# Performance work log

Measured on AMD Instinct MI355X. Metric: run time of the kernel, lower is better.

Reference implementation:

```python
import jax, jax.numpy as jnp
import numpy as np

M, N, IN, H, NC = 2048, 64, 16, 256, 64
OUT = 3 * NC
NUM_LAYERS = 2


def _lstm_layer(x, Wih, Whh, bih, bhh):
    # x: (M, T, F); Wih: (4H, F); Whh: (4H, H). Torch gate order: i, f, g, o.
    xg = jnp.einsum('mtf,gf->mtg', x, Wih) + bih + bhh  # (M, T, 4H)
    h0 = jnp.zeros((x.shape[0], Whh.shape[1]), x.dtype)

    def step(carry, xt):
        h, c = carry
        gates = xt + h @ Whh.T
        i, f, g, o = jnp.split(gates, 4, axis=-1)
        c = jax.nn.sigmoid(f) * c + jax.nn.sigmoid(i) * jnp.tanh(g)
        h = jax.nn.sigmoid(o) * jnp.tanh(c)
        return (h, c), h

    (_, _), hs = jax.lax.scan(step, (h0, h0), jnp.swapaxes(xg, 0, 1))
    return jnp.swapaxes(hs, 0, 1)  # (M, T, H)


def setup_inputs() -> dict:
    key = jax.random.key(0)
    ks = jax.random.split(key, 12)
    s = 1.0 / np.sqrt(H)
    d = {
        'z': jax.random.normal(ks[0], (M, N, IN), jnp.float32),
        'Wih0': jax.random.normal(ks[1], (4 * H, IN), jnp.float32) * s,
        'Whh0': jax.random.normal(ks[2], (4 * H, H), jnp.float32) * s,
        'bih0': jax.random.normal(ks[3], (4 * H,), jnp.float32) * s,
        'bhh0': jax.random.normal(ks[4], (4 * H,), jnp.float32) * s,
        'Wih1': jax.random.normal(ks[5], (4 * H, H), jnp.float32) * s,
        'Whh1': jax.random.normal(ks[6], (4 * H, H), jnp.float32) * s,
        'bih1': jax.random.normal(ks[7], (4 * H,), jnp.float32) * s,
        'bhh1': jax.random.normal(ks[8], (4 * H,), jnp.float32) * s,
        'fcW': jax.random.normal(ks[9], (OUT, H), jnp.float32) * 0.02,
        'fcb': jax.random.normal(ks[10], (OUT,), jnp.float32) * 0.02,
    }
    return d


def reference(z, Wih0, Whh0, bih0, bhh0, Wih1, Whh1, bih1, bhh1, fcW, fcb):
    h = _lstm_layer(z, Wih0, Whh0, bih0, bhh0)
    h = _lstm_layer(h, Wih1, Whh1, bih1, bhh1)
    y = jnp.einsum('mth,oh->mto', h, fcW) + fcb  # (M, N, 3*NC)

    gammas = jax.nn.softmax(y[..., :NC], axis=2)
    sigmas = jnp.exp(y[..., NC:2 * NC])
    mus = y[..., 2 * NC:]

    key = jax.random.key(42)
    k1, k2 = jax.random.split(key)
    idx = jax.random.categorical(k1, jnp.log(gammas), axis=-1)  # (M, N)
    chosen_mu = jnp.take_along_axis(mus, idx[..., None], axis=2)     # (M, N, 1)
    chosen_sig = jnp.take_along_axis(sigmas, idx[..., None], axis=2)
    eps = jax.random.normal(k2, chosen_mu.shape, jnp.float32)
    x_pred = jax.lax.stop_gradient(chosen_mu + chosen_sig * eps)  # Normal.sample (no grad)

    kern_exp = (x_pred - mus) ** 2                         # broadcast repeat over NC
    kernels = jnp.exp(-0.5 * kern_exp) / sigmas ** 2
    kernels = kernels / ((2.0 * jnp.pi) ** (N / 2) * sigmas ** N)
    x_cond_prob = jnp.einsum('mtc,mtc->mt', gammas, kernels)  # (M, N)
    return x_pred, x_cond_prob
```

## Files before the change

### kernel.cpp

```cpp
#include <hip/hip_runtime.h>
#include <stdint.h>
#include <stddef.h>

#define Mdim 2048
#define Tdim 64
#define INdim 16
#define Hdim 256
#define NCdim 64
#define NUG 64
#define HSLAB (256 * 2048)
#define RSLOTS 16

typedef __attribute__((ext_vector_type(8))) short s16x8;
typedef __attribute__((ext_vector_type(4))) float f32x4;

#define PANEL_US (3 * 16 * 8 * 512)
#define SPOFF 65536
#define BFRAG_US (3 * 8 * 3 * 512)

#define OFF_BFRAG 0
#define OFF_WZ    1179648
#define OFF_BB    (OFF_WZ + 64 * 256)
#define OFF_WFCP  (OFF_BB + 64 * 32)
#define OFF_H0P   (OFF_WFCP + 256 * 64 * 4)
#define OFF_C0    (OFF_H0P + 1572864)
#define OFF_C1    (OFF_C0 + HSLAB)
#define OFF_RINGF (OFF_C1 + HSLAB)
#define OFF_RING2 (OFF_RINGF + 12582912)
#define WS_TOT    (OFF_RING2 + RSLOTS * HSLAB)

#define ROTL32(v, s) (((v) << (s)) | ((v) >> (32 - (s))))

__host__ __device__ inline void tf2x32(uint32_t k0, uint32_t k1, uint32_t x0, uint32_t x1,
                                       uint32_t* o0, uint32_t* o1) {
  uint32_t ks2 = k0 ^ k1 ^ 0x1BD11BDAu;
  x0 += k0; x1 += k1;
  x0 += x1; x1 = ROTL32(x1, 13); x1 ^= x0;
  x0 += x1; x1 = ROTL32(x1, 15); x1 ^= x0;
  x0 += x1; x1 = ROTL32(x1, 26); x1 ^= x0;
  x0 += x1; x1 = ROTL32(x1, 6);  x1 ^= x0;
  x0 += k1; x1 += ks2 + 1u;
  x0 += x1; x1 = ROTL32(x1, 17); x1 ^= x0;
  x0 += x1; x1 = ROTL32(x1, 29); x1 ^= x0;
  x0 += x1; x1 = ROTL32(x1, 16); x1 ^= x0;
  x0 += x1; x1 = ROTL32(x1, 24); x1 ^= x0;
  x0 += ks2; x1 += k0 + 2u;
  x0 += x1; x1 = ROTL32(x1, 13); x1 ^= x0;
  x0 += x1; x1 = ROTL32(x1, 15); x1 ^= x0;
  x0 += x1; x1 = ROTL32(x1, 26); x1 ^= x0;
  x0 += x1; x1 = ROTL32(x1, 6);  x1 ^= x0;
  x0 += k0; x1 += k1 + 3u;
  x0 += x1; x1 = ROTL32(x1, 17); x1 ^= x0;
  x0 += x1; x1 = ROTL32(x1, 29); x1 ^= x0;
  x0 += x1; x1 = ROTL32(x1, 16); x1 ^= x0;
  x0 += x1; x1 = ROTL32(x1, 24); x1 ^= x0;
  x0 += k1; x1 += ks2 + 4u;
  x0 += x1; x1 = ROTL32(x1, 13); x1 ^= x0;
  x0 += x1; x1 = ROTL32(x1, 15); x1 ^= x0;
  x0 += x1; x1 = ROTL32(x1, 26); x1 ^= x0;
  x0 += x1; x1 = ROTL32(x1, 6);  x1 ^= x0;
  x0 += ks2; x1 += k0 + 5u;
  *o0 = x0; *o1 = x1;
}

__device__ inline uint32_t random_bits32(uint32_t ka, uint32_t kb, uint32_t p) {
  uint32_t a, b;
  tf2x32(ka, kb, 0u, p, &a, &b);
  return a ^ b;
}

__device__ inline float bits_to_u01(uint32_t bits) {
  return __uint_as_float((bits >> 9) | 0x3f800000u) - 1.0f;
}

__device__ inline float sigm_fast(float x) { return 1.0f / (1.0f + __expf(-x)); }

__device__ inline float erfinv_f32(float x) {
  float w = -log1pf(-x * x);
  float p;
  if (w < 5.0f) {
    w -= 2.5f;
    p = 2.81022636e-08f;
    p = fmaf(p, w, 3.43273939e-07f);
    p = fmaf(p, w, -3.5233877e-06f);
    p = fmaf(p, w, -4.39150654e-06f);
    p = fmaf(p, w, 0.00021858087f);
    p = fmaf(p, w, -0.00125372503f);
    p = fmaf(p, w, -0.00417768164f);
    p = fmaf(p, w, 0.246640727f);
    p = fmaf(p, w, 1.50140941f);
  } else {
    w = sqrtf(w) - 3.0f;
    p = -0.000200214257f;
    p = fmaf(p, w, 0.000100950558f);
    p = fmaf(p, w, 0.00134934322f);
    p = fmaf(p, w, -0.00367342844f);
    p = fmaf(p, w, 0.00573950773f);
    p = fmaf(p, w, -0.0076224613f);
    p = fmaf(p, w, 0.00943887047f);
    p = fmaf(p, w, 1.00167406f);
    p = fmaf(p, w, 2.83297682f);
  }
  return p * x;
}

__device__ inline void mdn_head(float yg, float ysg, float ym, int lane, uint32_t rid,
                                uint32_t k1a, uint32_t k1b, uint32_t k2a, uint32_t k2b,
                                float* __restrict__ out) {
  uint32_t pp = rid * (uint32_t)NCdim + (uint32_t)lane;
  uint32_t bits = random_bits32(k1a, k1b, pp);
  float u01 = bits_to_u01(bits);
  const float tinyf = 1.17549435e-38f;
  float uu = fmaxf(tinyf, u01 + tinyf);
  float gum = -logf(-logf(uu));
  float val = gum + yg;
  int idx = lane;
#pragma unroll
  for (int s = 1; s < 64; s <<= 1) {
    float ov = __shfl_xor(val, s);
    int oi = __shfl_xor(idx, s);
    if (ov > val || (ov == val && oi < idx)) { val = ov; idx = oi; }
  }
  float mu_sel = __shfl(ym, idx);
  float s_sel = __shfl(ysg, idx);

  uint32_t ebits = random_bits32(k2a, k2b, rid);
  float ue = bits_to_u01(ebits);
  const float lo = __uint_as_float(0xBF7FFFFFu);
  float un2 = fmaxf(lo, ue * 2.0f + lo);
  float eps = 1.41421356f * erfinv_f32(un2);

  float x_pred = mu_sel + expf(s_sel) * eps;

  float mx = yg;
#pragma unroll
  for (int s = 1; s < 64; s <<= 1) mx = fmaxf(mx, __shfl_xor(mx, s));
  float se = expf(yg - mx);
#pragma unroll
  for (int s = 1; s < 64; s <<= 1) se += __shfl_xor(se, s);
  float d = x_pred - ym;
  float lk = -0.5f * d * d - 66.0f * ysg - 58.812066f;
  float ts = expf(yg - mx + lk);
#pragma unroll
  for (int s = 1; s < 64; s <<= 1) ts += __shfl_xor(ts, s);
  float prob = ts / se;

  if (lane == 0) {
    out[rid] = x_pred;
    out[(size_t)Mdim * Tdim + rid] = prob;
  }
}

__device__ __host__ inline unsigned short bf16_trunc(float x) {
  union { float f; uint32_t u; } c; c.f = x;
  return (unsigned short)(c.u >> 16);
}
__device__ __host__ inline float bf16_tof(unsigned short s) {
  union { float f; uint32_t u; } c; c.u = ((uint32_t)s) << 16;
  return c.f;
}

__global__ void vfpg_prep(const float* __restrict__ Wih0, const float* __restrict__ Whh0,
                          const float* __restrict__ Wih1, const float* __restrict__ Whh1,
                          const float* __restrict__ fcW, const float* __restrict__ bih0,
                          const float* __restrict__ bhh0, const float* __restrict__ bih1,
                          const float* __restrict__ bhh1, float* __restrict__ ws) {
  int i0 = blockIdx.x * blockDim.x + threadIdx.x;
  int n = blockDim.x * gridDim.x;
  unsigned short* BF = (unsigned short*)(ws + OFF_BFRAG);
  for (int i = i0; i < 64 * 3 * 8 * 512; i += n) {
    int ug = i / 12288, r = i % 12288;
    int cls = r / 4096, r2 = r % 4096;
    int kt = r2 >> 9, pos = r2 & 511;
    int l = pos >> 3, e = pos & 7;
    int n16 = l & 15, lg = l >> 4;
    int k = kt * 32 + lg * 8 + e;
    int ul = n16 >> 2, ty = n16 & 3;
    int gd = ty * 256 + ug * 4 + ul;
    const float* W = (cls == 0) ? Whh0 : ((cls == 1) ? Wih1 : Whh1);
    float w = W[gd * 256 + k];
    unsigned short s0 = bf16_trunc(w);
    float r1 = w - bf16_tof(s0);
    unsigned short s1 = bf16_trunc(r1);
    unsigned short s2 = bf16_trunc(r1 - bf16_tof(s1));
    size_t base = ((size_t)(ug * 3 + cls) * 8 + kt) * (3 * 512) + pos;
    BF[base] = s0;
    BF[base + 512] = s1;
    BF[base + 1024] = s2;
  }
  for (int i = i0; i < 64 * 256; i += n) {
    int ug = i >> 8, k = (i >> 4) & 15, g = i & 15;
    int gd = (g & 3) * 256 + ug * 4 + (g >> 2);
    ws[OFF_WZ + i] = Wih0[gd * INdim + k];
  }
  for (int i = i0; i < 64 * 32; i += n) {
    int ug = i >> 5, r = i & 31, g = r & 15;
    int gd = (g & 3) * 256 + ug * 4 + (g >> 2);
    ws[OFF_BB + i] = (r < 16) ? (bih0[gd] + bhh0[gd]) : (bih1[gd] + bhh1[gd]);
  }
  float4* wfcp = (float4*)(ws + OFF_WFCP);
  for (int o = i0; o < 256 * 64; o += n) {
    int k = o >> 6, c = o & 63;
    wfcp[o] = make_float4(fcW[c * Hdim + k], fcW[(64 + c) * Hdim + k],
                          fcW[(128 + c) * Hdim + k], 0.0f);
  }
}

__device__ inline void cell1s(float gi, float gf, float gg, float go, float cold,
                              float* cn, float* hn) {
  float si = sigm_fast(gi), sf = sigm_fast(gf);
  float tg = fmaf(2.0f, sigm_fast(2.0f * gg), -1.0f);
  float so = sigm_fast(go);
  float cc = fmaf(sf, cold, si * tg);
  *cn = cc;
  *hn = so * fmaf(2.0f, sigm_fast(2.0f * cc), -1.0f);
}

#define GBS 17

template <int MODE>
__launch_bounds__(256, 3)
__global__ void vfpg_step(const float* __restrict__ z, const float* __restrict__ ws,
                          float* __restrict__ wsm, int t) {
  __shared__ unsigned short lB[2 * 8 * 2 * 512];
  __shared__ float gbuf[256 * GBS];
  __shared__ float lz[256];
  __shared__ float lbias[32];

  const int tid = threadIdx.x;
  const int rg = blockIdx.x & 7, ug = blockIdx.x >> 3;
  const int mb = rg * 256;
  const int lane = tid & 63, wid = tid >> 6;

  {
    const unsigned short* BG = (const unsigned short*)(ws + OFF_BFRAG) + (size_t)ug * BFRAG_US;
    s16x8* dst = (s16x8*)lB;
    for (int i = tid; i < 2 * 8 * 2 * 64; i += 256) {
      int ck = i >> 7, sp = (i >> 6) & 1, v = i & 63;
      dst[i] = *(const s16x8*)(BG + ((size_t)ck * 3 + sp) * 512 + v * 8);
    }
    if (tid < 64) ((float4*)lz)[tid] = ((const float4*)(ws + OFF_WZ + ug * 256))[tid];
    if (tid < 32) lbias[tid] = ws[OFF_BB + ug * 32 + tid];
  }
  __syncthreads();

  f32x4 aL0[4], aL1[4];
#pragma unroll
  for (int i = 0; i < 4; i++) {
    aL0[i] = (f32x4)0.0f;
    aL1[i] = (f32x4)0.0f;
  }

  if (MODE >= 1) {
    const unsigned short* p0 = (const unsigned short*)(ws + OFF_H0P) +
                               ((size_t)((t - 1) & 1) * 8 + rg) * PANEL_US;
    const unsigned short* p1 = (const unsigned short*)(ws + OFF_RINGF) +
                               ((size_t)((t - 2) & 15) * 8 + rg) * PANEL_US;
    const unsigned short* BG2 = (const unsigned short*)(ws + OFF_BFRAG) + (size_t)ug * BFRAG_US;
    const bool doH1 = (t >= 2);
    const s16x8* pLB = (const s16x8*)lB;

    s16x8 Ab0[6], Ab1[6];
    {
      size_t fb = ((size_t)(wid * 4) * 8 + 0) * 512 + lane * 8;
      Ab0[0] = *(const s16x8*)(p0 + fb);
      Ab0[1] = *(const s16x8*)(p0 + fb + SPOFF);
      Ab0[2] = *(const s16x8*)(p0 + fb + 2 * SPOFF);
      if (doH1) {
        Ab0[3] = *(const s16x8*)(p1 + fb);
        Ab0[4] = *(const s16x8*)(p1 + fb + SPOFF);
        Ab0[5] = *(const s16x8*)(p1 + fb + 2 * SPOFF);
      }
    }

#pragma unroll 1
    for (int kt = 0; kt < 8; kt++) {
      s16x8 bL0s0, bL0s1, bL0s2, bIs0, bIs1, bIs2, bHs0, bHs1, bHs2;
      if (MODE == 1) {
        bL0s0 = pLB[(kt * 2 + 0) * 64 + lane];
        bL0s1 = pLB[(kt * 2 + 1) * 64 + lane];
        bL0s2 = *(const s16x8*)(BG2 + ((size_t)kt * 3 + 2) * 512 + lane * 8);
      }
      bIs0 = pLB[((8 + kt) * 2 + 0) * 64 + lane];
      bIs1 = pLB[((8 + kt) * 2 + 1) * 64 + lane];
      bIs2 = *(const s16x8*)(BG2 + ((size_t)(8 + kt) * 3 + 2) * 512 + lane * 8);
      if (doH1) {
        bHs0 = *(const s16x8*)(BG2 + ((size_t)(16 + kt) * 3 + 0) * 512 + lane * 8);
        bHs1 = *(const s16x8*)(BG2 + ((size_t)(16 + kt) * 3 + 1) * 512 + lane * 8);
        bHs2 = *(const s16x8*)(BG2 + ((size_t)(16 + kt) * 3 + 2) * 512 + lane * 8);
      }
#pragma unroll
      for (int i = 0; i < 4; i++) {
        s16x8* cur = (i & 1) ? Ab1 : Ab0;
        s16x8* nxt = (i & 1) ? Ab0 : Ab1;
        int nkt = (i < 3) ? kt : kt + 1;
        int ni = (i < 3) ? (i + 1) : 0;
        if (nkt < 8) {
          size_t fb = ((size_t)(wid * 4 + ni) * 8 + nkt) * 512 + lane * 8;
          nxt[0] = *(const s16x8*)(p0 + fb);
          nxt[1] = *(const s16x8*)(p0 + fb + SPOFF);
          nxt[2] = *(const s16x8*)(p0 + fb + 2 * SPOFF);
          if (doH1) {
            nxt[3] = *(const s16x8*)(p1 + fb);
            nxt[4] = *(const s16x8*)(p1 + fb + SPOFF);
            nxt[5] = *(const s16x8*)(p1 + fb + 2 * SPOFF);
          }
        }
        s16x8 a0 = cur[0], a1 = cur[1], a2 = cur[2];
        if (MODE == 1) {
          aL0[i] = __builtin_amdgcn_mfma_f32_16x16x32_bf16(a0, bL0s0, aL0[i], 0, 0, 0);
          aL0[i] = __builtin_amdgcn_mfma_f32_16x16x32_bf16(a0, bL0s1, aL0[i], 0, 0, 0);
          aL0[i] = __builtin_amdgcn_mfma_f32_16x16x32_bf16(a1, bL0s0, aL0[i], 0, 0, 0);
          aL0[i] = __builtin_amdgcn_mfma_f32_16x16x32_bf16(a1, bL0s1, aL0[i], 0, 0, 0);
          aL0[i] = __builtin_amdgcn_mfma_f32_16x16x32_bf16(a0, bL0s2, aL0[i], 0, 0, 0);
          aL0[i] = __builtin_amdgcn_mfma_f32_16x16x32_bf16(a2, bL0s0, aL0[i], 0, 0, 0);
        }
        aL1[i] = __builtin_amdgcn_mfma_f32_16x16x32_bf16(a0, bIs0, aL1[i], 0, 0, 0);
        aL1[i] = __builtin_amdgcn_mfma_f32_16x16x32_bf16(a0, bIs1, aL1[i], 0, 0, 0);
        aL1[i] = __builtin_amdgcn_mfma_f32_16x16x32_bf16(a1, bIs0, aL1[i], 0, 0, 0);
        aL1[i] = __builtin_amdgcn_mfma_f32_16x16x32_bf16(a1, bIs1, aL1[i], 0, 0, 0);
        aL1[i] = __builtin_amdgcn_mfma_f32_16x16x32_bf16(a0, bIs2, aL1[i], 0, 0, 0);
        aL1[i] = __builtin_amdgcn_mfma_f32_16x16x32_bf16(a2, bIs0, aL1[i], 0, 0, 0);
        if (doH1) {
          s16x8 c0 = cur[3], c1 = cur[4], c2 = cur[5];
          aL1[i] = __builtin_amdgcn_mfma_f32_16x16x32_bf16(c0, bHs0, aL1[i], 0, 0, 0);
          aL1[i] = __builtin_amdgcn_mfma_f32_16x16x32_bf16(c0, bHs1, aL1[i], 0, 0, 0);
          aL1[i] = __builtin_amdgcn_mfma_f32_16x16x32_bf16(c1, bHs0, aL1[i], 0, 0, 0);
          aL1[i] = __builtin_amdgcn_mfma_f32_16x16x32_bf16(c1, bHs1, aL1[i], 0, 0, 0);
          aL1[i] = __builtin_amdgcn_mfma_f32_16x16x32_bf16(c0, bHs2, aL1[i], 0, 0, 0);
          aL1[i] = __builtin_amdgcn_mfma_f32_16x16x32_bf16(c2, bHs0, aL1[i], 0, 0, 0);
        }
      }
    }
  }

  float* c0w = wsm + OFF_C0;
  float* c1w = wsm + OFF_C1;
  const int mloc = tid;
  const int m = mb + mloc;
  const int mtc = mloc >> 4, mrowc = mloc & 15;
  const int ktw = ug >> 3;
  const int lgw = (ug & 7) >> 1;
  const int ebase = (ug * 4) & 7;
  const int lww = lgw * 16 + mrowc;
  const size_t fo = ((size_t)mtc * 8 + ktw) * 512 + lww * 8 + ebase;

  if (MODE <= 1) {
    if (MODE == 1) {
      int col = lane & 15, rb2 = (lane >> 4) * 4;
#pragma unroll
      for (int i = 0; i < 4; i++) {
        int mt = wid * 4 + i;
#pragma unroll
        for (int j = 0; j < 4; j++)
          gbuf[(mt * 16 + rb2 + j) * GBS + col] = aL0[i][j];
      }
    }
    __syncthreads();
    float zr[16];
#pragma unroll
    for (int f4 = 0; f4 < 4; f4++)
      *(float4*)&zr[f4 * 4] = *(const float4*)&z[(size_t)m * 1024 + t * 16 + f4 * 4];
    float g16[16];
#pragma unroll
    for (int gg = 0; gg < 16; gg++)
      g16[gg] = lbias[gg] + ((MODE == 1) ? gbuf[mloc * GBS + gg] : 0.0f);
#pragma unroll
    for (int f = 0; f < 16; f++) {
      float zv = zr[f];
      float4 w0 = *(const float4*)&lz[f * 16 + 0];
      float4 w1 = *(const float4*)&lz[f * 16 + 4];
      float4 w2 = *(const float4*)&lz[f * 16 + 8];
      float4 w3 = *(const float4*)&lz[f * 16 + 12];
      g16[0] = fmaf(zv, w0.x, g16[0]);  g16[1] = fmaf(zv, w0.y, g16[1]);
      g16[2] = fmaf(zv, w0.z, g16[2]);  g16[3] = fmaf(zv, w0.w, g16[3]);
      g16[4] = fmaf(zv, w1.x, g16[4]);  g16[5] = fmaf(zv, w1.y, g16[5]);
      g16[6] = fmaf(zv, w1.z, g16[6]);  g16[7] = fmaf(zv, w1.w, g16[7]);
      g16[8] = fmaf(zv, w2.x, g16[8]);  g16[9] = fmaf(zv, w2.y, g16[9]);
      g16[10] = fmaf(zv, w2.z, g16[10]); g16[11] = fmaf(zv, w2.w, g16[11]);
      g16[12] = fmaf(zv, w3.x, g16[12]); g16[13] = fmaf(zv, w3.y, g16[13]);
      g16[14] = fmaf(zv, w3.z, g16[14]); g16[15] = fmaf(zv, w3.w, g16[15]);
    }
    unsigned short* wp = (unsigned short*)(wsm + OFF_H0P) +
                         ((size_t)(t & 1) * 8 + rg) * PANEL_US;
    short sp0[4], sp1[4], sp2[4];
#pragma unroll
    for (int ul = 0; ul < 4; ul++) {
      int u = ug * 4 + ul;
      size_t cidx = (size_t)u * 2048 + m;
      float cold = (MODE == 1) ? c0w[cidx] : 0.0f;
      float cn, hn;
      cell1s(g16[ul * 4 + 0], g16[ul * 4 + 1], g16[ul * 4 + 2], g16[ul * 4 + 3], cold, &cn, &hn);
      c0w[cidx] = cn;
      unsigned short s0 = bf16_trunc(hn);
      float r1 = hn - bf16_tof(s0);
      unsigned short s1 = bf16_trunc(r1);
      unsigned short s2 = bf16_trunc(r1 - bf16_tof(s1));
      sp0[ul] = (short)s0; sp1[ul] = (short)s1; sp2[ul] = (short)s2;
    }
    *(short4*)&wp[fo]             = make_short4(sp0[0], sp0[1], sp0[2], sp0[3]);
    *(short4*)&wp[fo + SPOFF]     = make_short4(sp1[0], sp1[1], sp1[2], sp1[3]);
    *(short4*)&wp[fo + 2 * SPOFF] = make_short4(sp2[0], sp2[1], sp2[2], sp2[3]);
    __syncthreads();
  }

  if (MODE >= 1) {
    {
      int col = lane & 15, rb2 = (lane >> 4) * 4;
#pragma unroll
      for (int i = 0; i < 4; i++) {
        int mt = wid * 4 + i;
#pragma unroll
        for (int j = 0; j < 4; j++)
          gbuf[(mt * 16 + rb2 + j) * GBS + col] = aL1[i][j];
      }
    }
    __syncthreads();
    int slot = (t - 1) & 15;
    unsigned short* rp = (unsigned short*)(wsm + OFF_RINGF) +
                         ((size_t)slot * 8 + rg) * PANEL_US;
    float* r2 = wsm + OFF_RING2 + (size_t)slot * HSLAB;
    float h4[4];
    short sp0[4], sp1[4], sp2[4];
#pragma unroll
    for (int ul = 0; ul < 4; ul++) {
      int gg = ul * 4;
      float gi = lbias[16 + gg + 0] + gbuf[mloc * GBS + gg + 0];
      float gf = lbias[16 + gg + 1] + gbuf[mloc * GBS + gg + 1];
      float gt = lbias[16 + gg + 2] + gbuf[mloc * GBS + gg + 2];
      float go = lbias[16 + gg + 3] + gbuf[mloc * GBS + gg + 3];
      int u = ug * 4 + ul;
      size_t cidx = (size_t)u * 2048 + m;
      float cold = (t >= 2) ? c1w[cidx] : 0.0f;
      float cn, hn;
      cell1s(gi, gf, gt, go, cold, &cn, &hn);
      c1w[cidx] = cn;
      h4[ul] = hn;
      unsigned short s0 = bf16_trunc(hn);
      float r1v = hn - bf16_tof(s0);
      unsigned short s1 = bf16_trunc(r1v);
      unsigned short s2 = bf16_trunc(r1v - bf16_tof(s1));
      sp0[ul] = (short)s0; sp1[ul] = (short)s1; sp2[ul] = (short)s2;
    }
    *(short4*)&rp[fo]             = make_short4(sp0[0], sp0[1], sp0[2], sp0[3]);
    *(short4*)&rp[fo + SPOFF]     = make_short4(sp1[0], sp1[1], sp1[2], sp1[3]);
    *(short4*)&rp[fo + 2 * SPOFF] = make_short4(sp2[0], sp2[1], sp2[2], sp2[3]);
    *(float4*)&r2[(size_t)m * 256 + ug * 4] = make_float4(h4[0], h4[1], h4[2], h4[3]);
  }
}

__launch_bounds__(512, 2)
__global__ void vfpg_head(const float* __restrict__ ws, const float* __restrict__ fcb,
                          float* __restrict__ out, int tbase,
                          uint32_t k1a, uint32_t k1b, uint32_t k2a, uint32_t k2b) {
  __shared__ __align__(16) float hsw[8][8][Hdim];
  const int tid = threadIdx.x;
  const int lane = tid & 63, wid = tid >> 6;
  const int rb8 = blockIdx.x * 8 + wid;
  const int slot = rb8 >> 8;
  const int mbase = (rb8 & 255) * 8;

  const float* r2 = ws + OFF_RING2 + (size_t)slot * HSLAB + (size_t)mbase * 256;
  const float4* WFCP = (const float4*)(ws + OFF_WFCP);

#pragma unroll
  for (int rr = 0; rr < 8; rr++)
    *(float4*)&hsw[wid][rr][lane * 4] = *(const float4*)&r2[rr * 256 + lane * 4];
  __builtin_amdgcn_s_waitcnt(0);

  float yg[8], ys[8], ym[8];
#pragma unroll
  for (int rr = 0; rr < 8; rr++) {
    yg[rr] = fcb[lane]; ys[rr] = fcb[64 + lane]; ym[rr] = fcb[128 + lane];
  }
#pragma unroll 2
  for (int k4 = 0; k4 < 64; k4++) {
    float4 h4[8];
#pragma unroll
    for (int rr = 0; rr < 8; rr++) h4[rr] = *(const float4*)&hsw[wid][rr][k4 * 4];
#pragma unroll
    for (int j = 0; j < 4; j++) {
      float4 w = WFCP[(k4 * 4 + j) * 64 + lane];
#pragma unroll
      for (int rr = 0; rr < 8; rr++) {
        float hv = (&h4[rr].x)[j];
        yg[rr] = fmaf(hv, w.x, yg[rr]);
        ys[rr] = fmaf(hv, w.y, ys[rr]);
        ym[rr] = fmaf(hv, w.z, ym[rr]);
      }
    }
  }
  int tt = tbase + slot;
#pragma unroll 1
  for (int rr = 0; rr < 8; rr++) {
    uint32_t rid = (uint32_t)(mbase + rr) * Tdim + (uint32_t)tt;
    mdn_head(yg[rr], ys[rr], ym[rr], lane, rid, k1a, k1b, k2a, k2b, out);
  }
}

extern "C" void kernel_launch(void* const* d_in, const int* in_sizes, int n_in,
                              void* d_out, int out_size, void* d_ws, size_t ws_size,
                              hipStream_t stream) {
  const float* z    = (const float*)d_in[0];
  const float* Wih0 = (const float*)d_in[1];
  const float* Whh0 = (const float*)d_in[2];
  const float* bih0 = (const float*)d_in[3];
  const float* bhh0 = (const float*)d_in[4];
  const float* Wih1 = (const float*)d_in[5];
  const float* Whh1 = (const float*)d_in[6];
  const float* bih1 = (const float*)d_in[7];
  const float* bhh1 = (const float*)d_in[8];
  const float* fcW  = (const float*)d_in[9];
  const float* fcb  = (const float*)d_in[10];
  float* ws = (float*)d_ws;
  float* out = (float*)d_out;

  if (ws_size < (size_t)WS_TOT * sizeof(float)) return;

  vfpg_prep<<<dim3(512), dim3(256), 0, stream>>>(
      Wih0, Whh0, Wih1, Whh1, fcW, bih0, bhh0, bih1, bhh1, ws);

  uint32_t k1a, k1b, k2a, k2b;
  tf2x32(0u, 42u, 0u, 0u, &k1a, &k1b);
  tf2x32(0u, 42u, 0u, 1u, &k2a, &k2b);

  vfpg_step<0><<<dim3(512), dim3(256), 0, stream>>>(z, ws, ws, 0);
  for (int t = 1; t <= 63; t++) {
    vfpg_step<1><<<dim3(512), dim3(256), 0, stream>>>(z, ws, ws, t);
    if (t == 16 || t == 32 || t == 48) {
      vfpg_head<<<dim3(512), dim3(512), 0, stream>>>(ws, fcb, out, t - 16,
                                                     k1a, k1b, k2a, k2b);
    }
  }
  vfpg_step<2><<<dim3(512), dim3(256), 0, stream>>>(z, ws, ws, 64);
  vfpg_head<<<dim3(512), dim3(512), 0, stream>>>(ws, fcb, out, 48, k1a, k1b, k2a, k2b);
}
```

Baseline: 2.081 ms.

## Merge two unit-groups per block so A panels are reused across gate columns

Each step block now handles two unit-groups (512 threads, 256 blocks) instead of one, so every A-fragment load from the hidden-state panels feeds MFMAs for both groups. This halves global A traffic per output. All B fragments, including the split-2 and recurrent-layer-1 weights that were previously read from global each k-step, are now staged in shared memory through a union buffer reused for the gate scratch. The cost is higher shared-memory use (about 130 KB per block), fewer and larger blocks, lower occupancy, and an extra barrier before the gate buffer is reused.

After: 2.069 ms. About the same (-0.6%).

```diff
diff --git a/kernel.cpp b/kernel.cpp
--- a/kernel.cpp
+++ b/kernel.cpp
@@ -216,53 +216,67 @@
   *hn = so * fmaf(2.0f, sigm_fast(2.0f * cc), -1.0f);
 }
 
-#define GBS 17
+#define GBS2 33
 
 template <int MODE>
-__launch_bounds__(256, 3)
+__launch_bounds__(512, 2)
 __global__ void vfpg_step(const float* __restrict__ z, const float* __restrict__ ws,
                           float* __restrict__ wsm, int t) {
-  __shared__ unsigned short lB[2 * 8 * 2 * 512];
-  __shared__ float gbuf[256 * GBS];
-  __shared__ float lz[256];
-  __shared__ float lbias[32];
+  __shared__ unsigned short lB01[2 * 2 * 8 * 2 * 512];
+  __shared__ __align__(16) unsigned char uni[81920];
+  __shared__ float lz[2 * 256];
+  __shared__ float lbias[64];
 
   const int tid = threadIdx.x;
-  const int rg = blockIdx.x & 7, ug = blockIdx.x >> 3;
+  const int rg = blockIdx.x & 7, ugc = blockIdx.x >> 3;
   const int mb = rg * 256;
   const int lane = tid & 63, wid = tid >> 6;
+  float* gbuf = (float*)uni;
 
   {
-    const unsigned short* BG = (const unsigned short*)(ws + OFF_BFRAG) + (size_t)ug * BFRAG_US;
-    s16x8* dst = (s16x8*)lB;
-    for (int i = tid; i < 2 * 8 * 2 * 64; i += 256) {
-      int ck = i >> 7, sp = (i >> 6) & 1, v = i & 63;
-      dst[i] = *(const s16x8*)(BG + ((size_t)ck * 3 + sp) * 512 + v * 8);
-    }
-    if (tid < 64) ((float4*)lz)[tid] = ((const float4*)(ws + OFF_WZ + ug * 256))[tid];
-    if (tid < 32) lbias[tid] = ws[OFF_BB + ug * 32 + tid];
+    const unsigned short* BF = (const unsigned short*)(ws + OFF_BFRAG);
+    const unsigned short* BG0 = BF + (size_t)(ugc * 2 + 0) * BFRAG_US;
+    const unsigned short* BG1 = BF + (size_t)(ugc * 2 + 1) * BFRAG_US;
+    for (int i = tid; i < 2 * 4608; i += 512) {
+      int ugl = i / 4608;
+      int r = i % 4608;
+      int cls = r / 1536;
+      int r2 = r % 1536;
+      int kt = r2 / 192;
+      int sp = (r2 / 64) % 3;
+      int v = r2 & 63;
+      const unsigned short* src = (ugl ? BG1 : BG0) + ((size_t)(cls * 8 + kt) * 3 + sp) * 512 + v * 8;
+      s16x8 val = *(const s16x8*)src;
+      if (cls < 2 && sp < 2) {
+        ((s16x8*)lB01)[((((ugl * 2 + cls) * 8 + kt) * 2 + sp)) * 64 + v] = val;
+      } else {
+        int str = (cls == 2) ? (2 + sp) : cls;
+        ((s16x8*)uni)[(((ugl * 5 + str) * 8 + kt)) * 64 + v] = val;
+      }
+    }
+    if (tid < 128) ((float4*)lz)[tid] = ((const float4*)(ws + OFF_WZ + (ugc * 2) * 256))[tid];
+    if (tid < 64) lbias[tid] = ws[OFF_BB + (ugc * 2) * 32 + tid];
   }
   __syncthreads();
 
-  f32x4 aL0[4], aL1[4];
-#pragma unroll
-  for (int i = 0; i < 4; i++) {
-    aL0[i] = (f32x4)0.0f;
-    aL1[i] = (f32x4)0.0f;
-  }
+  f32x4 aL0[2][2], aL1[2][2];
+#pragma unroll
+  for (int i = 0; i < 2; i++)
+#pragma unroll
+    for (int u = 0; u < 2; u++) { aL0[i][u] = (f32x4)0.0f; aL1[i][u] = (f32x4)0.0f; }
 
   if (MODE >= 1) {
     const unsigned short* p0 = (const unsigned short*)(ws + OFF_H0P) +
                                ((size_t)((t - 1) & 1) * 8 + rg) * PANEL_US;
     const unsigned short* p1 = (const unsigned short*)(ws + OFF_RINGF) +
                                ((size_t)((t - 2) & 15) * 8 + rg) * PANEL_US;
-    const unsigned short* BG2 = (const unsigned short*)(ws + OFF_BFRAG) + (size_t)ug * BFRAG_US;
     const bool doH1 = (t >= 2);
-    const s16x8* pLB = (const s16x8*)lB;
+    const s16x8* pL = (const s16x8*)lB01;
+    const s16x8* pU = (const s16x8*)uni;
 
     s16x8 Ab0[6], Ab1[6];
     {
-      size_t fb = ((size_t)(wid * 4) * 8 + 0) * 512 + lane * 8;
+      size_t fb = ((size_t)(wid * 2) * 8 + 0) * 512 + lane * 8;
       Ab0[0] = *(const s16x8*)(p0 + fb);
       Ab0[1] = *(const s16x8*)(p0 + fb + SPOFF);
       Ab0[2] = *(const s16x8*)(p0 + fb + 2 * SPOFF);
@@ -275,28 +289,31 @@
 
 #pragma unroll 1
     for (int kt = 0; kt < 8; kt++) {
-      s16x8 bL0s0, bL0s1, bL0s2, bIs0, bIs1, bIs2, bHs0, bHs1, bHs2;
-      if (MODE == 1) {
-        bL0s0 = pLB[(kt * 2 + 0) * 64 + lane];
-        bL0s1 = pLB[(kt * 2 + 1) * 64 + lane];
-        bL0s2 = *(const s16x8*)(BG2 + ((size_t)kt * 3 + 2) * 512 + lane * 8);
+      s16x8 bL0s0[2], bL0s1[2], bL0s2[2], bIs0[2], bIs1[2], bIs2[2], bHs0[2], bHs1[2], bHs2[2];
+#pragma unroll
+      for (int u = 0; u < 2; u++) {
+        if (MODE == 1) {
+          bL0s0[u] = pL[(((u * 2 + 0) * 8 + kt) * 2 + 0) * 64 + lane];
+          bL0s1[u] = pL[(((u * 2 + 0) * 8 + kt) * 2 + 1) * 64 + lane];
+          bL0s2[u] = pU[((u * 5 + 0) * 8 + kt) * 64 + lane];
+        }
+        bIs0[u] = pL[(((u * 2 + 1) * 8 + kt) * 2 + 0) * 64 + lane];
+        bIs1[u] = pL[(((u * 2 + 1) * 8 + kt) * 2 + 1) * 64 + lane];
+        bIs2[u] = pU[((u * 5 + 1) * 8 + kt) * 64 + lane];
+        if (doH1) {
+          bHs0[u] = pU[((u * 5 + 2) * 8 + kt) * 64 + lane];
+          bHs1[u] = pU[((u * 5 + 3) * 8 + kt) * 64 + lane];
+          bHs2[u] = pU[((u * 5 + 4) * 8 + kt) * 64 + lane];
+        }
       }
-      bIs0 = pLB[((8 + kt) * 2 + 0) * 64 + lane];
-      bIs1 = pLB[((8 + kt) * 2 + 1) * 64 + lane];
-      bIs2 = *(const s16x8*)(BG2 + ((size_t)(8 + kt) * 3 + 2) * 512 + lane * 8);
-      if (doH1) {
-        bHs0 = *(const s16x8*)(BG2 + ((size_t)(16 + kt) * 3 + 0) * 512 + lane * 8);
-        bHs1 = *(const s16x8*)(BG2 + ((size_t)(16 + kt) * 3 + 1) * 512 + lane * 8);
-        bHs2 = *(const s16x8*)(BG2 + ((size_t)(16 + kt) * 3 + 2) * 512 + lane * 8);
-      }
-#pragma unroll
-      for (int i = 0; i < 4; i++) {
+#pragma unroll
+      for (int i = 0; i < 2; i++) {
         s16x8* cur = (i & 1) ? Ab1 : Ab0;
         s16x8* nxt = (i & 1) ? Ab0 : Ab1;
-        int nkt = (i < 3) ? kt : kt + 1;
-        int ni = (i < 3) ? (i + 1) : 0;
+        int nkt = (i < 1) ? kt : kt + 1;
+        int ni = (i < 1) ? 1 : 0;
         if (nkt < 8) {
-          size_t fb = ((size_t)(wid * 4 + ni) * 8 + nkt) * 512 + lane * 8;
+          size_t fb = ((size_t)(wid * 2 + ni) * 8 + nkt) * 512 + lane * 8;
           nxt[0] = *(const s16x8*)(p0 + fb);
           nxt[1] = *(const s16x8*)(p0 + fb + SPOFF);
           nxt[2] = *(const s16x8*)(p0 + fb + 2 * SPOFF);
@@ -307,37 +324,43 @@
           }
         }
         s16x8 a0 = cur[0], a1 = cur[1], a2 = cur[2];
-        if (MODE == 1) {
-          aL0[i] = __builtin_amdgcn_mfma_f32_16x16x32_bf16(a0, bL0s0, aL0[i], 0, 0, 0);
-          aL0[i] = __builtin_amdgcn_mfma_f32_16x16x32_bf16(a0, bL0s1, aL0[i], 0, 0, 0);
-          aL0[i] = __builtin_amdgcn_mfma_f32_16x16x32_bf16(a1, bL0s0, aL0[i], 0, 0, 0);
-          aL0[i] = __builtin_amdgcn_mfma_f32_16x16x32_bf16(a1, bL0s1, aL0[i], 0, 0, 0);
-          aL0[i] = __builtin_amdgcn_mfma_f32_16x16x32_bf16(a0, bL0s2, aL0[i], 0, 0, 0);
-          aL0[i] = __builtin_amdgcn_mfma_f32_16x16x32_bf16(a2, bL0s0, aL0[i], 0, 0, 0);
-        }
-        aL1[i] = __builtin_amdgcn_mfma_f32_16x16x32_bf16(a0, bIs0, aL1[i], 0, 0, 0);
-        aL1[i] = __builtin_amdgcn_mfma_f32_16x16x32_bf16(a0, bIs1, aL1[i], 0, 0, 0);
-        aL1[i] = __builtin_amdgcn_mfma_f32_16x16x32_bf16(a1, bIs0, aL1[i], 0, 0, 0);
-        aL1[i] = __builtin_amdgcn_mfma_f32_16x16x32_bf16(a1, bIs1, aL1[i], 0, 0, 0);
-        aL1[i] = __builtin_amdgcn_mfma_f32_16x16x32_bf16(a0, bIs2, aL1[i], 0, 0, 0);
-        aL1[i] = __builtin_amdgcn_mfma_f32_16x16x32_bf16(a2, bIs0, aL1[i], 0, 0, 0);
-        if (doH1) {
-          s16x8 c0 = cur[3], c1 = cur[4], c2 = cur[5];
-          aL1[i] = __builtin_amdgcn_mfma_f32_16x16x32_bf16(c0, bHs0, aL1[i], 0, 0, 0);
-          aL1[i] = __builtin_amdgcn_mfma_f32_16x16x32_bf16(c0, bHs1, aL1[i], 0, 0, 0);
-          aL1[i] = __builtin_amdgcn_mfma_f32_16x16x32_bf16(c1, bHs0, aL1[i], 0, 0, 0);
-          aL1[i] = __builtin_amdgcn_mfma_f32_16x16x32_bf16(c1, bHs1, aL1[i], 0, 0, 0);
-          aL1[i] = __builtin_amdgcn_mfma_f32_16x16x32_bf16(c0, bHs2, aL1[i], 0, 0, 0);
-          aL1[i] = __builtin_amdgcn_mfma_f32_16x16x32_bf16(c2, bHs0, aL1[i], 0, 0, 0);
+#pragma unroll
+        for (int u = 0; u < 2; u++) {
+          if (MODE == 1) {
+            aL0[i][u] = __builtin_amdgcn_mfma_f32_16x16x32_bf16(a0, bL0s0[u], aL0[i][u], 0, 0, 0);
+            aL0[i][u] = __builtin_amdgcn_mfma_f32_16x16x32_bf16(a0, bL0s1[u], aL0[i][u], 0, 0, 0);
+            aL0[i][u] = __builtin_amdgcn_mfma_f32_16x16x32_bf16(a1, bL0s0[u], aL0[i][u], 0, 0, 0);
+            aL0[i][u] = __builtin_amdgcn_mfma_f32_16x16x32_bf16(a1, bL0s1[u], aL0[i][u], 0, 0, 0);
+            aL0[i][u] = __builtin_amdgcn_mfma_f32_16x16x32_bf16(a0, bL0s2[u], aL0[i][u], 0, 0, 0);
+            aL0[i][u] = __builtin_amdgcn_mfma_f32_16x16x32_bf16(a2, bL0s0[u], aL0[i][u], 0, 0, 0);
+          }
+          aL1[i][u] = __builtin_amdgcn_mfma_f32_16x16x32_bf16(a0, bIs0[u], aL1[i][u], 0, 0, 0);
+          aL1[i][u] = __builtin_amdgcn_mfma_f32_16x16x32_bf16(a0, bIs1[u], aL1[i][u], 0, 0, 0);
+          aL1[i][u] = __builtin_amdgcn_mfma_f32_16x16x32_bf16(a1, bIs0[u], aL1[i][u], 0, 0, 0);
+          aL1[i][u] = __builtin_amdgcn_mfma_f32_16x16x32_bf16(a1, bIs1[u], aL1[i][u], 0, 0, 0);
+          aL1[i][u] = __builtin_amdgcn_mfma_f32_16x16x32_bf16(a0, bIs2[u], aL1[i][u], 0, 0, 0);
+          aL1[i][u] = __builtin_amdgcn_mfma_f32_16x16x32_bf16(a2, bIs0[u], aL1[i][u], 0, 0, 0);
+          if (doH1) {
+            s16x8 c0 = cur[3], c1 = cur[4], c2 = cur[5];
+            aL1[i][u] = __builtin_amdgcn_mfma_f32_16x16x32_bf16(c0, bHs0[u], aL1[i][u], 0, 0, 0);
+            aL1[i][u] = __builtin_amdgcn_mfma_f32_16x16x32_bf16(c0, bHs1[u], aL1[i][u], 0, 0, 0);
+            aL1[i][u] = __builtin_amdgcn_mfma_f32_16x16x32_bf16(c1, bHs0[u], aL1[i][u], 0, 0, 0);
+            aL1[i][u] = __builtin_amdgcn_mfma_f32_16x16x32_bf16(c1, bHs1[u], aL1[i][u], 0, 0, 0);
+            aL1[i][u] = __builtin_amdgcn_mfma_f32_16x16x32_bf16(c0, bHs2[u], aL1[i][u], 0, 0, 0);
+            aL1[i][u] = __builtin_amdgcn_mfma_f32_16x16x32_bf16(c2, bHs0[u], aL1[i][u], 0, 0, 0);
+          }
         }
       }
     }
   }
+  __syncthreads();
 
   float* c0w = wsm + OFF_C0;
   float* c1w = wsm + OFF_C1;
-  const int mloc = tid;
+  const int ugl = tid >> 8;
+  const int mloc = tid & 255;
   const int m = mb + mloc;
+  const int ug = ugc * 2 + ugl;
   const int mtc = mloc >> 4, mrowc = mloc & 15;
   const int ktw = ug >> 3;
   const int lgw = (ug & 7) >> 1;
@@ -349,12 +372,12 @@
     if (MODE == 1) {
       int col = lane & 15, rb2 = (lane >> 4) * 4;
 #pragma unroll
-      for (int i = 0; i < 4; i++) {
-        int mt = wid * 4 + i;
-#pragma unroll
-        for (int j = 0; j < 4; j++)
-          gbuf[(mt * 16 + rb2 + j) * GBS + col] = aL0[i][j];
-      }
+      for (int i = 0; i < 2; i++)
+#pragma unroll
+        for (int u = 0; u < 2; u++)
+#pragma unroll
+          for (int j = 0; j < 4; j++)
+            gbuf[((wid * 2 + i) * 16 + rb2 + j) * GBS2 + u * 16 + col] = aL0[i][u][j];
     }
     __syncthreads();
     float zr[16];
@@ -364,14 +387,15 @@
     float g16[16];
 #pragma unroll
     for (int gg = 0; gg < 16; gg++)
-      g16[gg] = lbias[gg] + ((MODE == 1) ? gbuf[mloc * GBS + gg] : 0.0f);
+      g16[gg] = lbias[ugl * 32 + gg] + ((MODE == 1) ? gbuf[mloc * GBS2 + ugl * 16 + gg] : 0.0f);
+    const float* lzu = lz + ugl * 256;
 #pragma unroll
     for (int f = 0; f < 16; f++) {
       float zv = zr[f];
-      float4 w0 = *(const float4*)&lz[f * 16 + 0];
-      float4 w1 = *(const float4*)&lz[f * 16 + 4];
-      float4 w2 = *(const float4*)&lz[f * 16 + 8];
-      float4 w3 = *(const float4*)&lz[f * 16 + 12];
+      float4 w0 = *(const float4*)&lzu[f * 16 + 0];
+      float4 w1 = *(const float4*)&lzu[f * 16 + 4];
+      float4 w2 = *(const float4*)&lzu[f * 16 + 8];
+      float4 w3 = *(const float4*)&lzu[f * 16 + 12];
       g16[0] = fmaf(zv, w0.x, g16[0]);  g16[1] = fmaf(zv, w0.y, g16[1]);
       g16[2] = fmaf(zv, w0.z, g16[2]);  g16[3] = fmaf(zv, w0.w, g16[3]);
       g16[4] = fmaf(zv, w1.x, g16[4]);  g16[5] = fmaf(zv, w1.y, g16[5]);
@@ -408,12 +432,12 @@
     {
       int col = lane & 15, rb2 = (lane >> 4) * 4;
 #pragma unroll
-      for (int i = 0; i < 4; i++) {
-        int mt = wid * 4 + i;
-#pragma unroll
-        for (int j = 0; j < 4; j++)
-          gbuf[(mt * 16 + rb2 + j) * GBS + col] = aL1[i][j];
-      }
+      for (int i = 0; i < 2; i++)
+#pragma unroll
+        for (int u = 0; u < 2; u++)
+#pragma unroll
+          for (int j = 0; j < 4; j++)
+            gbuf[((wid * 2 + i) * 16 + rb2 + j) * GBS2 + u * 16 + col] = aL1[i][u][j];
     }
     __syncthreads();
     int slot = (t - 1) & 15;
@@ -424,11 +448,10 @@
     short sp0[4], sp1[4], sp2[4];
 #pragma unroll
     for (int ul = 0; ul < 4; ul++) {
-      int gg = ul * 4;
-      float gi = lbias[16 + gg + 0] + gbuf[mloc * GBS + gg + 0];
-      float gf = lbias[16 + gg + 1] + gbuf[mloc * GBS + gg + 1];
-      float gt = lbias[16 + gg + 2] + gbuf[mloc * GBS + gg + 2];
-      float go = lbias[16 + gg + 3] + gbuf[mloc * GBS + gg + 3];
+      float gi = lbias[ugl * 32 + 16 + ul * 4 + 0] + gbuf[mloc * GBS2 + ugl * 16 + ul * 4 + 0];
+      float gf = lbias[ugl * 32 + 16 + ul * 4 + 1] + gbuf[mloc * GBS2 + ugl * 16 + ul * 4 + 1];
+      float gt = lbias[ugl * 32 + 16 + ul * 4 + 2] + gbuf[mloc * GBS2 + ugl * 16 + ul * 4 + 2];
+      float go = lbias[ugl * 32 + 16 + ul * 4 + 3] + gbuf[mloc * GBS2 + ugl * 16 + ul * 4 + 3];
       int u = ug * 4 + ul;
       size_t cidx = (size_t)u * 2048 + m;
       float cold = (t >= 2) ? c1w[cidx] : 0.0f;
@@ -524,14 +547,14 @@
   tf2x32(0u, 42u, 0u, 0u, &k1a, &k1b);
   tf2x32(0u, 42u, 0u, 1u, &k2a, &k2b);
 
-  vfpg_step<0><<<dim3(512), dim3(256), 0, stream>>>(z, ws, ws, 0);
+  vfpg_step<0><<<dim3(256), dim3(512), 0, stream>>>(z, ws, ws, 0);
   for (int t = 1; t <= 63; t++) {
-    vfpg_step<1><<<dim3(512), dim3(256), 0, stream>>>(z, ws, ws, t);
+    vfpg_step<1><<<dim3(256), dim3(512), 0, stream>>>(z, ws, ws, t);
     if (t == 16 || t == 32 || t == 48) {
       vfpg_head<<<dim3(512), dim3(512), 0, stream>>>(ws, fcb, out, t - 16,
                                                      k1a, k1b, k2a, k2b);
     }
   }
-  vfpg_step<2><<<dim3(512), dim3(256), 0, stream>>>(z, ws, ws, 64);
+  vfpg_step<2><<<dim3(256), dim3(512), 0, stream>>>(z, ws, ws, 64);
   vfpg_head<<<dim3(512), dim3(512), 0, stream>>>(ws, fcb, out, 48, k1a, k1b, k2a, k2b);
 }
```
